# Performance work log

Hardware: AMD Instinct MI355X
Metric: run time of the kernel (lower is better)

The kernel has to match this reference:

```python
import jax, jax.numpy as jnp
import numpy as np

B, T, C = 4, 2048, 1024
H = 16
HS = C // H  # 64
FF = 4 * C
EPS = 1e-5


def setup_inputs() -> dict:
    key = jax.random.key(0)
    ks = jax.random.split(key, 12)
    s = lambda k, shape, fan: jax.random.normal(k, shape, jnp.float32) * (fan ** -0.5)
    return {
        "x": jax.random.normal(ks[0], (B, T, C), jnp.float32),
        "Wq": s(ks[1], (H, C, HS), C),
        "Wk": s(ks[2], (H, C, HS), C),
        "Wv": s(ks[3], (H, C, HS), C),
        "Wproj": s(ks[4], (C, C), C),
        "bproj": jnp.zeros((C,), jnp.float32),
        "W1": s(ks[5], (C, FF), C),
        "b1": jnp.zeros((FF,), jnp.float32),
        "W2": s(ks[6], (FF, C), FF),
        "b2": jnp.zeros((C,), jnp.float32),
        "g1": jnp.ones((C,), jnp.float32),
        "be1": jnp.zeros((C,), jnp.float32),
        "g2": jnp.ones((C,), jnp.float32),
        "be2": jnp.zeros((C,), jnp.float32),
    }


def _layernorm(x, g, b):
    mu = jnp.mean(x, axis=-1, keepdims=True)
    var = jnp.mean(jnp.square(x - mu), axis=-1, keepdims=True)
    return (x - mu) * jax.lax.rsqrt(var + EPS) * g + b


def reference(x, Wq, Wk, Wv, Wproj, bproj, W1, b1, W2, b2, g1, be1, g2, be2):
    # --- multi-head causal self-attention on ln1(x) ---
    h = _layernorm(x, g1, be1)                      # [B,T,C]
    q = jnp.einsum("btc,hcd->bhtd", h, Wq)
    k = jnp.einsum("btc,hcd->bhtd", h, Wk)
    v = jnp.einsum("btc,hcd->bhtd", h, Wv)
    scores = jnp.einsum("bhtd,bhsd->bhts", q, k) * (HS ** -0.5)  # [B,H,T,T]
    causal = jnp.tril(jnp.ones((T, T), bool))
    scores = jnp.where(causal, scores, -jnp.inf)
    wei = jax.nn.softmax(scores, axis=-1)
    attn = jnp.einsum("bhts,bhsd->bhtd", wei, v)    # [B,H,T,HS]
    attn = attn.transpose(0, 2, 1, 3).reshape(B, T, C)  # concat heads
    x = x + attn @ Wproj + bproj
    # --- feed-forward on ln2(x) ---
    h2 = _layernorm(x, g2, be2)
    x = x + jax.nn.relu(h2 @ W1 + b1) @ W2 + b2
    return x
```

## Files before the change

### kernel.cpp

```cpp
#include <hip/hip_runtime.h>
#include <hip/hip_bf16.h>
#include <stdint.h>


typedef unsigned short u16;
typedef __bf16 bf16x8 __attribute__((ext_vector_type(8)));
typedef float f32x4 __attribute__((ext_vector_type(4)));
typedef float f32x16 __attribute__((ext_vector_type(16)));

#define MFMA16(a, b, c) __builtin_amdgcn_mfma_f32_16x16x32_bf16((a), (b), (c), 0, 0, 0)
#define MFMA32(a, b, c) __builtin_amdgcn_mfma_f32_32x32x16_bf16((a), (b), (c), 0, 0, 0)

__device__ __forceinline__ u16 f2bf(float f) {
  __hip_bfloat16 h = __float2bfloat16(f);
  return __builtin_bit_cast(u16, h);
}

__device__ __forceinline__ float bf2f(u16 u) {
  uint32_t t = (uint32_t)u << 16;
  return __builtin_bit_cast(float, t);
}

__device__ __forceinline__ uint32_t cvtpk(float lo, float hi_) {
  uint32_t r;
  asm("v_cvt_pk_bf16_f32 %0, %1, %2" : "=v"(r) : "v"(lo), "v"(hi_));
  return r;
}

__device__ __forceinline__ void pl32swap(uint32_t& a, uint32_t& b) {
  asm("v_permlane32_swap_b32 %0, %1" : "+v"(a), "+v"(b));
}

__device__ __forceinline__ void gload16(const void* g, void* l) {
  __builtin_amdgcn_global_load_lds(
      (__attribute__((address_space(1))) void*)g,
      (__attribute__((address_space(3))) void*)l, 16, 0, 0);
}

__device__ __forceinline__ void ln_body(
    int row, int tid, const float* __restrict__ x, const float* __restrict__ g,
    const float* __restrict__ be, u16* __restrict__ out, float* red) {
  const float4 v = reinterpret_cast<const float4*>(x + (size_t)row * 1024)[tid];
  float s = v.x + v.y + v.z + v.w;
  float s2 = v.x * v.x + v.y * v.y + v.z * v.z + v.w * v.w;
#pragma unroll
  for (int off = 1; off < 64; off <<= 1) {
    s += __shfl_xor(s, off);
    s2 += __shfl_xor(s2, off);
  }
  const int wid = tid >> 6;
  if ((tid & 63) == 0) { red[wid] = s; red[4 + wid] = s2; }
  __syncthreads();
  s = red[0] + red[1] + red[2] + red[3];
  s2 = red[4] + red[5] + red[6] + red[7];
  const float mu = s * (1.0f / 1024.0f);
  const float rstd = rsqrtf(s2 * (1.0f / 1024.0f) - mu * mu + 1e-5f);
  const float4 gv = reinterpret_cast<const float4*>(g)[tid];
  const float4 bv = reinterpret_cast<const float4*>(be)[tid];
  ushort4 o;
  o.x = f2bf((v.x - mu) * rstd * gv.x + bv.x);
  o.y = f2bf((v.y - mu) * rstd * gv.y + bv.y);
  o.z = f2bf((v.z - mu) * rstd * gv.z + bv.z);
  o.w = f2bf((v.w - mu) * rstd * gv.w + bv.w);
  *reinterpret_cast<ushort4*>(out + (size_t)row * 1024 + tid * 4) = o;
}

__global__ __launch_bounds__(256) void ln_kernel(
    const float* __restrict__ x, const float* __restrict__ g,
    const float* __restrict__ be, u16* __restrict__ out) {
  __shared__ float red[8];
  ln_body(blockIdx.x, threadIdx.x, x, g, be, out, red);
}

__global__ __launch_bounds__(256) void prep(
    const float* __restrict__ x, const float* __restrict__ g1,
    const float* __restrict__ be1, u16* __restrict__ hb,
    const float* __restrict__ Wq, const float* __restrict__ Wk,
    const float* __restrict__ Wv, const float* __restrict__ Wproj,
    const float* __restrict__ W1, const float* __restrict__ W2,
    u16* __restrict__ wqkvt, u16* __restrict__ wprojt,
    u16* __restrict__ w1t, u16* __restrict__ w2t) {
  __shared__ float t[64][65];
  const int tid = threadIdx.x;
  int b = blockIdx.x;
  if (b < 8192) {
    ln_body(b, tid, x, g1, be1, hb, &t[0][0]);
    return;
  }
  b -= 8192;
  const float* src;
  u16* dst;
  int R, C, bx, by;
  if (b < 768) {
    const int w = b >> 8, r = b & 255;
    const int z = r >> 4;
    src = (w == 0 ? Wq : w == 1 ? Wk : Wv) + (size_t)z * 65536;
    dst = wqkvt + w * 1048576 + (size_t)z * 65536;
    R = 1024; C = 64; bx = r & 15; by = 0;
  } else if (b < 1024) {
    const int r = b - 768;
    src = Wproj; dst = wprojt; R = 1024; C = 1024; bx = r & 15; by = r >> 4;
  } else if (b < 2048) {
    const int r = b - 1024;
    src = W1; dst = w1t; R = 1024; C = 4096; bx = r & 15; by = r >> 4;
  } else {
    const int r = b - 2048;
    src = W2; dst = w2t; R = 4096; C = 1024; bx = r & 63; by = r >> 6;
  }
  const int r0 = bx * 64, c0 = by * 64;
  const int cc = tid & 63, rr = tid >> 6;
#pragma unroll
  for (int p = 0; p < 16; ++p) {
    const int r = rr + p * 4;
    t[r][cc] = src[(size_t)(r0 + r) * C + c0 + cc];
  }
  __syncthreads();
#pragma unroll
  for (int p = 0; p < 16; ++p) {
    const int c = rr + p * 4;
    dst[(size_t)(c0 + c) * R + r0 + cc] = f2bf(t[cc][c]);
  }
}

__global__ __launch_bounds__(256) void ff2_combine(
    const u16* __restrict__ p0, const u16* __restrict__ p1,
    const float* __restrict__ b2, float* __restrict__ out) {
  const size_t base = ((size_t)blockIdx.x * 256 + threadIdx.x) * 8;
  const uint4 a0 = *reinterpret_cast<const uint4*>(p0 + base);
  const uint4 a1 = *reinterpret_cast<const uint4*>(p1 + base);
  const u16* e0 = reinterpret_cast<const u16*>(&a0);
  const u16* e1 = reinterpret_cast<const u16*>(&a1);
  const int c = (int)(base & 1023);
  const float4 bv0 = *reinterpret_cast<const float4*>(b2 + c);
  const float4 bv1 = *reinterpret_cast<const float4*>(b2 + c + 4);
  float4 o0 = *reinterpret_cast<const float4*>(out + base);
  float4 o1 = *reinterpret_cast<const float4*>(out + base + 4);
  o0.x += bf2f(e0[0]) + bf2f(e1[0]) + bv0.x;
  o0.y += bf2f(e0[1]) + bf2f(e1[1]) + bv0.y;
  o0.z += bf2f(e0[2]) + bf2f(e1[2]) + bv0.z;
  o0.w += bf2f(e0[3]) + bf2f(e1[3]) + bv0.w;
  o1.x += bf2f(e0[4]) + bf2f(e1[4]) + bv1.x;
  o1.y += bf2f(e0[5]) + bf2f(e1[5]) + bv1.y;
  o1.z += bf2f(e0[6]) + bf2f(e1[6]) + bv1.z;
  o1.w += bf2f(e0[7]) + bf2f(e1[7]) + bv1.w;
  *reinterpret_cast<float4*>(out + base) = o0;
  *reinterpret_cast<float4*>(out + base + 4) = o1;
}

constexpr int EPI_QKV = 0;
constexpr int EPI_RES = 1;
constexpr int EPI_RELU = 2;
constexpr int EPI_PART = 3;

template <int EPI>
__global__ __launch_bounds__(512) void gemm256(
    const u16* __restrict__ A, const u16* __restrict__ Bt,
    int M, int N, int Kloop, int Kstride, int NBN, int SPLIT,
    u16* outB, u16* outB2, float* outF, const float* bias) {
  __shared__ u16 sA[2][256 * 64] __attribute__((aligned(16)));
  __shared__ u16 sB[2][256 * 64] __attribute__((aligned(16)));
  const int tid = threadIdx.x;
  const int lane = tid & 63, wid = tid >> 6;
  const int wr = wid >> 2, wc = wid & 3;
  const int l16 = lane & 15, lg = lane >> 4;
  const int nwg = gridDim.x;
  const int wgid = (blockIdx.x & 7) * (nwg >> 3) + (blockIdx.x >> 3);
  int wg = wgid, ks = 0;
  if (SPLIT) { ks = wg & 1; wg >>= 1; }
  const int bm = wg / NBN, bn = wg % NBN;
  const u16* Ap = A + (size_t)ks * Kloop;
  const u16* Btp = Bt + (size_t)ks * Kloop;
  u16* outp = (SPLIT && ks) ? outB2 : outB;
  const size_t rowA = (size_t)bm * 256;
  const size_t rowB = (size_t)bn * 256;
  const int nkt = Kloop >> 6;

  f32x4 acc[8][4];
#pragma unroll
  for (int m = 0; m < 8; ++m)
#pragma unroll
    for (int n = 0; n < 4; ++n) {
      acc[m][n][0] = 0.f; acc[m][n][1] = 0.f; acc[m][n][2] = 0.f; acc[m][n][3] = 0.f;
    }

  auto stageA = [&](int kt, int h) {
    if (kt >= nkt) return;
    const int k0 = kt << 6;
    char* base = (char*)&sA[kt & 1][h * 8192];
#pragma unroll
    for (int it = 0; it < 2; ++it) {
      const int f = tid + it * 512;
      const int r = f >> 3, c = f & 7;
      gload16(Ap + (rowA + h * 128 + r) * Kstride + k0 + ((c ^ (r & 7)) << 3), base + f * 16);
    }
  };
  auto stageB = [&](int kt, int h) {
    if (kt >= nkt) return;
    const int k0 = kt << 6;
    char* base = (char*)&sB[kt & 1][h * 8192];
#pragma unroll
    for (int it = 0; it < 2; ++it) {
      const int f = tid + it * 512;
      const int r = f >> 3, c = f & 7;
      gload16(Btp + (rowB + h * 128 + r) * Kstride + k0 + ((c ^ (r & 7)) << 3), base + f * 16);
    }
  };

  stageA(0, 0); stageB(0, 0); stageA(0, 1); stageB(0, 1);
  stageB(1, 0); stageA(1, 0);
  asm volatile("s_waitcnt vmcnt(4)" ::: "memory");
  __builtin_amdgcn_s_barrier();
  asm volatile("" ::: "memory");

  bf16x8 a[4][2], b[4][2];
  for (int kt = 0; kt < nkt; ++kt) {
    const u16* bufA = &sA[kt & 1][0];
    const u16* bufB = &sB[kt & 1][0];
#pragma unroll
    for (int m = 0; m < 4; ++m)
#pragma unroll
      for (int kk = 0; kk < 2; ++kk) {
        const int r = wr * 128 + m * 16 + l16;
        a[m][kk] = *reinterpret_cast<const bf16x8*>(bufA + r * 64 + (((kk * 4 + lg) ^ (r & 7)) << 3));
      }
#pragma unroll
    for (int n = 0; n < 2; ++n)
#pragma unroll
      for (int kk = 0; kk < 2; ++kk) {
        const int r = wc * 64 + n * 16 + l16;
        b[n][kk] = *reinterpret_cast<const bf16x8*>(bufB + r * 64 + (((kk * 4 + lg) ^ (r & 7)) << 3));
      }
    stageB(kt + 1, 1);
    __builtin_amdgcn_s_barrier();
    asm volatile("s_waitcnt lgkmcnt(0)" ::: "memory");
    __builtin_amdgcn_s_setprio(1);
#pragma unroll
    for (int kk = 0; kk < 2; ++kk)
#pragma unroll
      for (int m = 0; m < 4; ++m)
#pragma unroll
        for (int n = 0; n < 2; ++n)
          acc[m][n] = MFMA16(a[m][kk], b[n][kk], acc[m][n]);
    __builtin_amdgcn_s_setprio(0);
    __builtin_amdgcn_s_barrier();
    asm volatile("" ::: "memory");
#pragma unroll
    for (int n = 2; n < 4; ++n)
#pragma unroll
      for (int kk = 0; kk < 2; ++kk) {
        const int r = wc * 64 + n * 16 + l16;
        b[n][kk] = *reinterpret_cast<const bf16x8*>(bufB + r * 64 + (((kk * 4 + lg) ^ (r & 7)) << 3));
      }
    stageA(kt + 1, 1);
    __builtin_amdgcn_s_barrier();
    asm volatile("s_waitcnt lgkmcnt(0)" ::: "memory");
    __builtin_amdgcn_s_setprio(1);
#pragma unroll
    for (int kk = 0; kk < 2; ++kk)
#pragma unroll
      for (int m = 0; m < 4; ++m)
#pragma unroll
        for (int n = 2; n < 4; ++n)
          acc[m][n] = MFMA16(a[m][kk], b[n][kk], acc[m][n]);
    __builtin_amdgcn_s_setprio(0);
    __builtin_amdgcn_s_barrier();
    asm volatile("" ::: "memory");
#pragma unroll
    for (int m = 0; m < 4; ++m)
#pragma unroll
      for (int kk = 0; kk < 2; ++kk) {
        const int r = wr * 128 + 64 + m * 16 + l16;
        a[m][kk] = *reinterpret_cast<const bf16x8*>(bufA + r * 64 + (((kk * 4 + lg) ^ (r & 7)) << 3));
      }
    stageB(kt + 2, 0);
    __builtin_amdgcn_s_barrier();
    asm volatile("s_waitcnt lgkmcnt(0)" ::: "memory");
    __builtin_amdgcn_s_setprio(1);
#pragma unroll
    for (int kk = 0; kk < 2; ++kk)
#pragma unroll
      for (int m = 0; m < 4; ++m)
#pragma unroll
        for (int n = 2; n < 4; ++n)
          acc[4 + m][n] = MFMA16(a[m][kk], b[n][kk], acc[4 + m][n]);
    __builtin_amdgcn_s_setprio(0);
    __builtin_amdgcn_s_barrier();
    asm volatile("" ::: "memory");
    stageA(kt + 2, 0);
    __builtin_amdgcn_s_setprio(1);
#pragma unroll
    for (int kk = 0; kk < 2; ++kk)
#pragma unroll
      for (int m = 0; m < 4; ++m)
#pragma unroll
        for (int n = 0; n < 2; ++n)
          acc[4 + m][n] = MFMA16(a[m][kk], b[n][kk], acc[4 + m][n]);
    __builtin_amdgcn_s_setprio(0);
    if (kt + 2 < nkt) {
      asm volatile("s_waitcnt vmcnt(4)" ::: "memory");
    } else {
      asm volatile("s_waitcnt vmcnt(0)" ::: "memory");
    }
    __builtin_amdgcn_s_barrier();
    asm volatile("" ::: "memory");
  }

#pragma unroll
  for (int m = 0; m < 8; ++m)
#pragma unroll
    for (int n = 0; n < 4; ++n)
#pragma unroll
      for (int ii = 0; ii < 4; ++ii) {
        const int gi = bm * 256 + wr * 128 + m * 16 + lg * 4 + ii;
        const int gj = bn * 256 + wc * 64 + n * 16 + l16;
        const float val = acc[m][n][ii];
        if constexpr (EPI == EPI_QKV) {
          const int sel = gj >> 10;
          const int hh = (gj >> 6) & 15;
          const int dd = gj & 63;
          const int bb = gi >> 11, tt = gi & 2047;
          const float sv = (sel == 0) ? val * 0.1803368801f : val;
          outB[(size_t)sel * 8388608 + ((size_t)(bb * 16 + hh) * 2048 + tt) * 64 + dd] = f2bf(sv);
        } else if constexpr (EPI == EPI_RELU) {
          const float bv = val + bias[gj];
          outB[(size_t)gi * N + gj] = f2bf(bv > 0.f ? bv : 0.f);
        } else if constexpr (EPI == EPI_PART) {
          outp[(size_t)gi * N + gj] = f2bf(val);
        }
      }
}

template <int EPI>
__global__ __launch_bounds__(512) void gemm128(
    const u16* __restrict__ A, const u16* __restrict__ Bt,
    int M, int N, int K, int NBN,
    u16* outB, float* outF, const float* bias, const float* res) {
  __shared__ u16 sA[2][128 * 64] __attribute__((aligned(16)));
  __shared__ u16 sB[2][256 * 64] __attribute__((aligned(16)));
  const int tid = threadIdx.x;
  const int lane = tid & 63, wid = tid >> 6;
  const int wr = wid >> 2, wc = wid & 3;
  const int l16 = lane & 15, lg = lane >> 4;
  const int nwg = gridDim.x;
  const int wgid = (blockIdx.x & 7) * (nwg >> 3) + (blockIdx.x >> 3);
  const int bm = wgid / NBN, bn = wgid % NBN;
  const size_t rowA = (size_t)bm * 128;
  const size_t rowB = (size_t)bn * 256;
  const int nkt = K >> 6;

  f32x4 acc[4][4];
#pragma unroll
  for (int m = 0; m < 4; ++m)
#pragma unroll
    for (int n = 0; n < 4; ++n) {
      acc[m][n][0] = 0.f; acc[m][n][1] = 0.f; acc[m][n][2] = 0.f; acc[m][n][3] = 0.f;
    }

  auto stageA = [&](int kt, int h) {
    if (kt >= nkt) return;
    const int k0 = kt << 6;
    char* base = (char*)&sA[kt & 1][h * 4096];
    const int r = tid >> 3, c = tid & 7;
    gload16(A + (rowA + h * 64 + r) * K + k0 + ((c ^ (r & 7)) << 3), base + tid * 16);
  };
  auto stageB = [&](int kt, int h) {
    if (kt >= nkt) return;
    const int k0 = kt << 6;
    char* base = (char*)&sB[kt & 1][h * 8192];
#pragma unroll
    for (int it = 0; it < 2; ++it) {
      const int f = tid + it * 512;
      const int r = f >> 3, c = f & 7;
      gload16(Bt + (rowB + h * 128 + r) * K + k0 + ((c ^ (r & 7)) << 3), base + f * 16);
    }
  };

  stageA(0, 0); stageB(0, 0); stageA(0, 1); stageB(0, 1);
  stageB(1, 0); stageA(1, 0);
  asm volatile("s_waitcnt vmcnt(3)" ::: "memory");
  __builtin_amdgcn_s_barrier();
  asm volatile("" ::: "memory");

  bf16x8 a[2][2], b[4][2];
  for (int kt = 0; kt < nkt; ++kt) {
    const u16* bufA = &sA[kt & 1][0];
    const u16* bufB = &sB[kt & 1][0];
#pragma unroll
    for (int m = 0; m < 2; ++m)
#pragma unroll
      for (int kk = 0; kk < 2; ++kk) {
        const int r = wr * 64 + m * 16 + l16;
        a[m][kk] = *reinterpret_cast<const bf16x8*>(bufA + r * 64 + (((kk * 4 + lg) ^ (r & 7)) << 3));
      }
#pragma unroll
    for (int n = 0; n < 2; ++n)
#pragma unroll
      for (int kk = 0; kk < 2; ++kk) {
        const int r = wc * 64 + n * 16 + l16;
        b[n][kk] = *reinterpret_cast<const bf16x8*>(bufB + r * 64 + (((kk * 4 + lg) ^ (r & 7)) << 3));
      }
    stageB(kt + 1, 1);
    __builtin_amdgcn_s_barrier();
    asm volatile("s_waitcnt lgkmcnt(0)" ::: "memory");
    __builtin_amdgcn_s_setprio(1);
#pragma unroll
    for (int kk = 0; kk < 2; ++kk)
#pragma unroll
      for (int m = 0; m < 2; ++m)
#pragma unroll
        for (int n = 0; n < 2; ++n)
          acc[m][n] = MFMA16(a[m][kk], b[n][kk], acc[m][n]);
    __builtin_amdgcn_s_setprio(0);
    __builtin_amdgcn_s_barrier();
    asm volatile("" ::: "memory");
#pragma unroll
    for (int n = 2; n < 4; ++n)
#pragma unroll
      for (int kk = 0; kk < 2; ++kk) {
        const int r = wc * 64 + n * 16 + l16;
        b[n][kk] = *reinterpret_cast<const bf16x8*>(bufB + r * 64 + (((kk * 4 + lg) ^ (r & 7)) << 3));
      }
    stageA(kt + 1, 1);
    __builtin_amdgcn_s_barrier();
    asm volatile("s_waitcnt lgkmcnt(0)" ::: "memory");
    __builtin_amdgcn_s_setprio(1);
#pragma unroll
    for (int kk = 0; kk < 2; ++kk)
#pragma unroll
      for (int m = 0; m < 2; ++m)
#pragma unroll
        for (int n = 2; n < 4; ++n)
          acc[m][n] = MFMA16(a[m][kk], b[n][kk], acc[m][n]);
    __builtin_amdgcn_s_setprio(0);
    __builtin_amdgcn_s_barrier();
    asm volatile("" ::: "memory");
#pragma unroll
    for (int m = 0; m < 2; ++m)
#pragma unroll
      for (int kk = 0; kk < 2; ++kk) {
        const int r = wr * 64 + (m + 2) * 16 + l16;
        a[m][kk] = *reinterpret_cast<const bf16x8*>(bufA + r * 64 + (((kk * 4 + lg) ^ (r & 7)) << 3));
      }
    stageB(kt + 2, 0);
    __builtin_amdgcn_s_barrier();
    asm volatile("s_waitcnt lgkmcnt(0)" ::: "memory");
    __builtin_amdgcn_s_setprio(1);
#pragma unroll
    for (int kk = 0; kk < 2; ++kk)
#pragma unroll
      for (int m = 0; m < 2; ++m)
#pragma unroll
        for (int n = 2; n < 4; ++n)
          acc[2 + m][n] = MFMA16(a[m][kk], b[n][kk], acc[2 + m][n]);
    __builtin_amdgcn_s_setprio(0);
    __builtin_amdgcn_s_barrier();
    asm volatile("" ::: "memory");
    stageA(kt + 2, 0);
    __builtin_amdgcn_s_setprio(1);
#pragma unroll
    for (int kk = 0; kk < 2; ++kk)
#pragma unroll
      for (int m = 0; m < 2; ++m)
#pragma unroll
        for (int n = 0; n < 2; ++n)
          acc[2 + m][n] = MFMA16(a[m][kk], b[n][kk], acc[2 + m][n]);
    __builtin_amdgcn_s_setprio(0);
    if (kt + 2 < nkt) {
      asm volatile("s_waitcnt vmcnt(3)" ::: "memory");
    } else {
      asm volatile("s_waitcnt vmcnt(0)" ::: "memory");
    }
    __builtin_amdgcn_s_barrier();
    asm volatile("" ::: "memory");
  }

#pragma unroll
  for (int m = 0; m < 4; ++m)
#pragma unroll
    for (int n = 0; n < 4; ++n)
#pragma unroll
      for (int ii = 0; ii < 4; ++ii) {
        const int gi = bm * 128 + wr * 64 + m * 16 + lg * 4 + ii;
        const int gj = bn * 256 + wc * 64 + n * 16 + l16;
        const float val = acc[m][n][ii];
        if constexpr (EPI == EPI_RES) {
          const size_t idx = (size_t)gi * N + gj;
          outF[idx] = val + bias[gj] + res[idx];
        }
      }
}

__device__ __constant__ int QTAB[16] = {15, 14, 13, 12, 11, 10, 9, 8,
                                        4, 5, 6, 7, 0, 1, 2, 3};

__global__ __launch_bounds__(256, 3) void attn_kernel(
    const u16* __restrict__ q, const u16* __restrict__ k,
    const u16* __restrict__ v, u16* __restrict__ o) {
  const int bid = blockIdx.x;
  const int bh = (bid & 7) * 8 + ((bid >> 3) & 7);
  const int qt = QTAB[bid >> 6];
  const int tid = threadIdx.x;
  const int lane = tid & 63, wid = tid >> 6;
  const int l32 = lane & 31, hi = lane >> 5;
  const u16* qb = q + (size_t)bh * (2048 * 64);
  const u16* kb = k + (size_t)bh * (2048 * 64);
  const u16* vb = v + (size_t)bh * (2048 * 64);
  const int q0 = qt * 128;
  const int qrow = q0 + wid * 32 + l32;

  __shared__ u16 sK[2][64 * 64] __attribute__((aligned(16)));
  __shared__ u16 sVt[2][64 * 72] __attribute__((aligned(16)));

  bf16x8 bq[4];
#pragma unroll
  for (int s = 0; s < 4; ++s)
    bq[s] = *reinterpret_cast<const bf16x8*>(qb + (size_t)qrow * 64 + s * 16 + hi * 8);

  bf16x8 aone;
  {
    union { u16 u[8]; bf16x8 v; } onec;
    const u16 ov = (l32 == 0) ? (u16)0x3F80 : (u16)0;
#pragma unroll
    for (int j = 0; j < 8; ++j) onec.u[j] = ov;
    aone = onec.v;
  }

  f32x16 oacc[2], osum;
#pragma unroll
  for (int r = 0; r < 16; ++r) { oacc[0][r] = 0.f; oacc[1][r] = 0.f; osum[r] = 0.f; }
  float mi = -1e30f;

  uint4 vr0, vr1;

  auto stageK = [&](int s0, int buf) {
#pragma unroll
    for (int it = 0; it < 2; ++it) {
      const int f = tid + it * 256;
      const int r = f >> 3, c = f & 7;
      gload16(kb + (size_t)(s0 + r) * 64 + (size_t)((c ^ (r & 7)) * 8),
              (char*)&sK[buf][0] + it * 4096 + wid * 1024);
    }
  };
  auto loadV = [&](int s0) {
    const int kvp = tid & 31;
    const int c8 = tid >> 5;
    vr0 = *reinterpret_cast<const uint4*>(vb + (size_t)(s0 + 2 * kvp) * 64 + c8 * 8);
    vr1 = *reinterpret_cast<const uint4*>(vb + (size_t)(s0 + 2 * kvp + 1) * 64 + c8 * 8);
  };
  auto writeV = [&](int buf) {
    const int kvp = tid & 31;
    const int c8 = tid >> 5;
    const u16* e0 = reinterpret_cast<const u16*>(&vr0);
    const u16* e1 = reinterpret_cast<const u16*>(&vr1);
    u16* base = &sVt[buf][0];
#pragma unroll
    for (int j = 0; j < 8; ++j) {
      const int d = c8 * 8 + j;
      *reinterpret_cast<uint32_t*>(base + d * 72 + 2 * kvp) =
          (uint32_t)e0[j] | ((uint32_t)e1[j] << 16);
    }
  };

  const int nst = 2 * qt + 2;
  stageK(0, 0);
  loadV(0);
  asm volatile("s_waitcnt vmcnt(0)" ::: "memory");
  writeV(0);
  __syncthreads();

  int cur = 0;
  for (int ks = 0; ks < nst; ++ks) {
    const int s0 = ks * 64;
    const int nxt = cur ^ 1;
    if (ks + 1 < nst) { stageK(s0 + 64, nxt); loadV(s0 + 64); }

    f32x16 st[2];
#pragma unroll
    for (int r = 0; r < 16; ++r) { st[0][r] = 0.f; st[1][r] = 0.f; }
#pragma unroll
    for (int t = 0; t < 2; ++t) {
      const int row = t * 32 + l32;
      const int rx = row & 7;
#pragma unroll
      for (int s = 0; s < 4; ++s) {
        bf16x8 ak = *reinterpret_cast<const bf16x8*>(
            &sK[cur][0] + row * 64 + (((s * 2 + hi) ^ rx) << 3));
        st[t] = MFMA32(ak, bq[s], st[t]);
      }
    }

    if (ks >= 2 * qt) {
#pragma unroll
      for (int t = 0; t < 2; ++t)
#pragma unroll
        for (int a = 0; a < 4; ++a)
#pragma unroll
          for (int c2 = 0; c2 < 4; ++c2) {
            const int kvg = s0 + t * 32 + a * 8 + hi * 4 + c2;
            if (kvg > qrow) st[t][a * 4 + c2] = -1e30f;
          }
    }

    float tm[16];
#pragma unroll
    for (int r = 0; r < 16; ++r) tm[r] = fmaxf(st[0][r], st[1][r]);
#pragma unroll
    for (int s2 = 8; s2 >= 1; s2 >>= 1)
#pragma unroll
      for (int r = 0; r < s2; ++r) tm[r] = fmaxf(tm[r], tm[r + s2]);
    const float pm = fmaxf(tm[0], __shfl_xor(tm[0], 32));
    if (__any(pm > mi)) {
      const float mn = fmaxf(mi, pm);
      const float al = exp2f(mi - mn);
      mi = mn;
      osum[0] *= al;
#pragma unroll
      for (int dt = 0; dt < 2; ++dt)
#pragma unroll
        for (int r = 0; r < 16; ++r) oacc[dt][r] *= al;
    }
#pragma unroll
    for (int t = 0; t < 2; ++t)
#pragma unroll
      for (int r = 0; r < 16; ++r) st[t][r] = exp2f(st[t][r] - mi);

    uint32_t W[2][4][2];
#pragma unroll
    for (int t = 0; t < 2; ++t)
#pragma unroll
      for (int a = 0; a < 4; ++a) {
        W[t][a][0] = cvtpk(st[t][a * 4 + 0], st[t][a * 4 + 1]);
        W[t][a][1] = cvtpk(st[t][a * 4 + 2], st[t][a * 4 + 3]);
      }
#pragma unroll
    for (int ks2 = 0; ks2 < 4; ++ks2) {
      const int t = ks2 >> 1;
      uint32_t A0 = W[t][(2 * ks2) & 3][0], B0 = W[t][(2 * ks2 + 1) & 3][0];
      uint32_t A1 = W[t][(2 * ks2) & 3][1], B1 = W[t][(2 * ks2 + 1) & 3][1];
      pl32swap(A0, B0);
      pl32swap(A1, B1);
      union { uint32_t w[4]; bf16x8 v; } bp;
      bp.w[0] = A0; bp.w[1] = A1; bp.w[2] = B0; bp.w[3] = B1;
#pragma unroll
      for (int dt = 0; dt < 2; ++dt) {
        bf16x8 av = *reinterpret_cast<const bf16x8*>(
            &sVt[cur][0] + (dt * 32 + l32) * 72 + ks2 * 16 + hi * 8);
        oacc[dt] = MFMA32(av, bp.v, oacc[dt]);
      }
      osum = MFMA32(aone, bp.v, osum);
    }

    if (ks + 1 < nst) {
      asm volatile("s_waitcnt vmcnt(0)" ::: "memory");
      writeV(nxt);
      __syncthreads();
    }
    cur = nxt;
  }

  const float li = __shfl(osum[0], l32);
  const int bb = bh >> 4, hh = bh & 15;
  const float rli = 1.0f / li;
  const size_t rowo = (size_t)(bb * 2048 + qrow) * 1024;
#pragma unroll
  for (int dt = 0; dt < 2; ++dt)
#pragma unroll
    for (int a = 0; a < 4; ++a) {
      ushort4 pk;
      pk.x = f2bf(oacc[dt][a * 4 + 0] * rli);
      pk.y = f2bf(oacc[dt][a * 4 + 1] * rli);
      pk.z = f2bf(oacc[dt][a * 4 + 2] * rli);
      pk.w = f2bf(oacc[dt][a * 4 + 3] * rli);
      *reinterpret_cast<ushort4*>(o + rowo + hh * 64 + dt * 32 + a * 8 + hi * 4) = pk;
    }
}

extern "C" void kernel_launch(void* const* d_in, const int* in_sizes, int n_in,
                              void* d_out, int out_size, void* d_ws, size_t ws_size,
                              hipStream_t stream) {
  const float* x = (const float*)d_in[0];
  const float* Wq = (const float*)d_in[1];
  const float* Wk = (const float*)d_in[2];
  const float* Wv = (const float*)d_in[3];
  const float* Wproj = (const float*)d_in[4];
  const float* bproj = (const float*)d_in[5];
  const float* W1 = (const float*)d_in[6];
  const float* b1 = (const float*)d_in[7];
  const float* W2 = (const float*)d_in[8];
  const float* b2 = (const float*)d_in[9];
  const float* g1 = (const float*)d_in[10];
  const float* be1 = (const float*)d_in[11];
  const float* g2 = (const float*)d_in[12];
  const float* be2 = (const float*)d_in[13];
  float* out = (float*)d_out;

  char* ws = (char*)d_ws;
  const size_t MB16 = 16777216ull;
  u16* hb = (u16*)(ws);
  u16* qkv = (u16*)(ws + MB16);
  u16* qp = qkv;
  u16* kp = qkv + 8388608;
  u16* vp = qkv + 2 * 8388608;
  u16* ab = (u16*)(ws + 4 * MB16);
  u16* f1 = qkv;
  u16* wqkvt = (u16*)(ws + 5 * MB16);
  u16* wprojt = wqkvt + 3145728;
  u16* w1t = wprojt + 1048576;
  u16* w2t = w1t + 4194304;
  u16* p0 = hb;
  u16* p1 = wqkvt;

  dim3 blk(256);
  prep<<<11264, blk, 0, stream>>>(x, g1, be1, hb, Wq, Wk, Wv, Wproj, W1, W2,
                                  wqkvt, wprojt, w1t, w2t);
  gemm256<EPI_QKV><<<384, 512, 0, stream>>>(hb, wqkvt, 8192, 3072, 1024, 1024, 12, 0,
                                            qkv, nullptr, nullptr, nullptr);
  attn_kernel<<<1024, blk, 0, stream>>>(qp, kp, vp, ab);
  gemm128<EPI_RES><<<256, 512, 0, stream>>>(ab, wprojt, 8192, 1024, 1024, 4,
                                            nullptr, out, bproj, x);
  ln_kernel<<<8192, blk, 0, stream>>>(out, g2, be2, hb);
  gemm256<EPI_RELU><<<512, 512, 0, stream>>>(hb, w1t, 8192, 4096, 1024, 1024, 16, 0,
                                             f1, nullptr, nullptr, b1);
  gemm256<EPI_PART><<<256, 512, 0, stream>>>(f1, w2t, 8192, 1024, 2048, 4096, 4, 1,
                                             p0, p1, nullptr, nullptr);
  ff2_combine<<<4096, blk, 0, stream>>>(p0, p1, b2, out);
}
```

Baseline: 364.4 us.

## Prefetch V two tiles ahead, add MFMA priority hints, raise attention occupancy

The attention kernel now loads V registers two KV tiles ahead using alternating register sets. It waits with vmcnt(2) instead of draining all loads, so global V latency overlaps more compute. It also wraps the QK and PV MFMA blocks in s_setprio(1)/s_setprio(0), and raises launch bounds to 4 blocks per CU. The extra V registers and the higher occupancy target may cause spills or register pressure. The vmcnt(2) count assumes exactly two outstanding V loads, with the async K loads already retired, which is fragile.

New measurement: 586.9 us. 1.61x slower.

```diff
diff --git a/kernel.cpp b/kernel.cpp
--- a/kernel.cpp
+++ b/kernel.cpp
@@ -493,7 +493,7 @@
 __device__ __constant__ int QTAB[16] = {15, 14, 13, 12, 11, 10, 9, 8,
                                         4, 5, 6, 7, 0, 1, 2, 3};
 
-__global__ __launch_bounds__(256, 3) void attn_kernel(
+__global__ __launch_bounds__(256, 4) void attn_kernel(
     const u16* __restrict__ q, const u16* __restrict__ k,
     const u16* __restrict__ v, u16* __restrict__ o) {
   const int bid = blockIdx.x;
@@ -530,7 +530,7 @@
   for (int r = 0; r < 16; ++r) { oacc[0][r] = 0.f; oacc[1][r] = 0.f; osum[r] = 0.f; }
   float mi = -1e30f;
 
-  uint4 vr0, vr1;
+  uint4 vA0, vA1, vB0, vB1;
 
   auto stageK = [&](int s0, int buf) {
 #pragma unroll
@@ -541,17 +541,17 @@
               (char*)&sK[buf][0] + it * 4096 + wid * 1024);
     }
   };
-  auto loadV = [&](int s0) {
+  auto loadV = [&](int s0, uint4& r0, uint4& r1) {
     const int kvp = tid & 31;
     const int c8 = tid >> 5;
-    vr0 = *reinterpret_cast<const uint4*>(vb + (size_t)(s0 + 2 * kvp) * 64 + c8 * 8);
-    vr1 = *reinterpret_cast<const uint4*>(vb + (size_t)(s0 + 2 * kvp + 1) * 64 + c8 * 8);
+    r0 = *reinterpret_cast<const uint4*>(vb + (size_t)(s0 + 2 * kvp) * 64 + c8 * 8);
+    r1 = *reinterpret_cast<const uint4*>(vb + (size_t)(s0 + 2 * kvp + 1) * 64 + c8 * 8);
   };
-  auto writeV = [&](int buf) {
+  auto writeV = [&](int buf, const uint4& r0, const uint4& r1) {
     const int kvp = tid & 31;
     const int c8 = tid >> 5;
-    const u16* e0 = reinterpret_cast<const u16*>(&vr0);
-    const u16* e1 = reinterpret_cast<const u16*>(&vr1);
+    const u16* e0 = reinterpret_cast<const u16*>(&r0);
+    const u16* e1 = reinterpret_cast<const u16*>(&r1);
     u16* base = &sVt[buf][0];
 #pragma unroll
     for (int j = 0; j < 8; ++j) {
@@ -563,20 +563,27 @@
 
   const int nst = 2 * qt + 2;
   stageK(0, 0);
-  loadV(0);
+  loadV(0, vA0, vA1);
   asm volatile("s_waitcnt vmcnt(0)" ::: "memory");
-  writeV(0);
+  writeV(0, vA0, vA1);
+  loadV(64, vB0, vB1);
   __syncthreads();
 
   int cur = 0;
   for (int ks = 0; ks < nst; ++ks) {
     const int s0 = ks * 64;
     const int nxt = cur ^ 1;
-    if (ks + 1 < nst) { stageK(s0 + 64, nxt); loadV(s0 + 64); }
+    const bool evn = (ks & 1) == 0;
+    if (ks + 1 < nst) stageK(s0 + 64, nxt);
+    if (ks + 2 < nst) {
+      if (evn) loadV(s0 + 128, vA0, vA1);
+      else loadV(s0 + 128, vB0, vB1);
+    }
 
     f32x16 st[2];
 #pragma unroll
     for (int r = 0; r < 16; ++r) { st[0][r] = 0.f; st[1][r] = 0.f; }
+    __builtin_amdgcn_s_setprio(1);
 #pragma unroll
     for (int t = 0; t < 2; ++t) {
       const int row = t * 32 + l32;
@@ -588,6 +595,7 @@
         st[t] = MFMA32(ak, bq[s], st[t]);
       }
     }
+    __builtin_amdgcn_s_setprio(0);
 
     if (ks >= 2 * qt) {
 #pragma unroll
@@ -632,6 +640,7 @@
         W[t][a][0] = cvtpk(st[t][a * 4 + 0], st[t][a * 4 + 1]);
         W[t][a][1] = cvtpk(st[t][a * 4 + 2], st[t][a * 4 + 3]);
       }
+    __builtin_amdgcn_s_setprio(1);
 #pragma unroll
     for (int ks2 = 0; ks2 < 4; ++ks2) {
       const int t = ks2 >> 1;
@@ -649,10 +658,16 @@
       }
       osum = MFMA32(aone, bp.v, osum);
     }
+    __builtin_amdgcn_s_setprio(0);
 
     if (ks + 1 < nst) {
-      asm volatile("s_waitcnt vmcnt(0)" ::: "memory");
-      writeV(nxt);
+      if (ks + 2 < nst) {
+        asm volatile("s_waitcnt vmcnt(2)" ::: "memory");
+      } else {
+        asm volatile("s_waitcnt vmcnt(0)" ::: "memory");
+      }
+      if (evn) writeV(nxt, vB0, vB1);
+      else writeV(nxt, vA0, vA1);
       __syncthreads();
     }
     cur = nxt;
```
